# Kernel optimization log

Measured on AMD Instinct MI355X. Metric: run time of the kernel, lower is better.

Reference implementation:

```python
import jax, jax.numpy as jnp
from jax import lax
import numpy as np

R = 500          # Resampling: temporal segment width
H = 100          # fixed signal height from the reshape in forward
EPS = 1e-5       # BatchNorm2d default eps
FLAT = 6 * 31 * 32


def _cbrp(x, w, b, g, be, m, v):
    """Conv(5x5, pad 2) + inference BatchNorm + ReLU + MaxPool 2x2."""
    x = lax.conv_general_dilated(x, w, (1, 1), ((2, 2), (2, 2)),
                                 dimension_numbers=('NCHW', 'OIHW', 'NCHW'))
    x = x + b[None, :, None, None]
    inv = g * lax.rsqrt(v + EPS)
    x = x * inv[None, :, None, None] + (be - m * inv)[None, :, None, None]
    x = jax.nn.relu(x)
    return lax.reduce_window(x, -jnp.inf, lax.max, (1, 1, 2, 2), (1, 1, 2, 2), 'VALID')


def setup_inputs() -> dict:
    key = jax.random.key(0)
    ks = jax.random.split(key, 16)
    d = {}
    d['x'] = jax.random.normal(ks[0], (16, 1, 100, 4000), dtype=jnp.float32)
    chans = [(1, 16), (16, 32), (32, 64), (64, 32)]
    for i, (ci, co) in enumerate(chans, start=1):
        fan_in = ci * 25
        d[f'w{i}'] = jax.random.normal(ks[i], (co, ci, 5, 5), dtype=jnp.float32) * np.float32((2.0 / fan_in) ** 0.5)
        d[f'b{i}'] = jnp.zeros((co,), jnp.float32)
        d[f'g{i}'] = jnp.ones((co,), jnp.float32)
        d[f'be{i}'] = jnp.zeros((co,), jnp.float32)
        d[f'm{i}'] = jnp.zeros((co,), jnp.float32)
        d[f'v{i}'] = jnp.ones((co,), jnp.float32)
    d['fw1'] = jax.random.normal(ks[5], (32, FLAT), dtype=jnp.float32) * np.float32(FLAT ** -0.5)
    d['fb1'] = jnp.zeros((32,), jnp.float32)
    d['fw2'] = jax.random.normal(ks[6], (2, 32), dtype=jnp.float32) * np.float32(32 ** -0.5)
    d['fb2'] = jnp.zeros((2,), jnp.float32)
    return d


def reference(x, w1, b1, g1, be1, m1, v1,
              w2, b2, g2, be2, m2, v2,
              w3, b3, g3, be3, m3, v3,
              w4, b4, g4, be4, m4, v4,
              fw1, fb1, fw2, fb2):
    B = x.shape[0]
    L = x.shape[-1] // R  # number of temporal segments per sample
    # (B,1,100,L*R) -> (B*L,1,100,R): batch all segments into one conv call
    xs = x[:, 0].reshape(B, H, L, R).transpose(0, 2, 1, 3).reshape(B * L, 1, H, R)
    h = _cbrp(xs, w1, b1, g1, be1, m1, v1)   # (BL,16,50,250)
    h = _cbrp(h, w2, b2, g2, be2, m2, v2)    # (BL,32,25,125)
    h = _cbrp(h, w3, b3, g3, be3, m3, v3)    # (BL,64,12,62)
    h = _cbrp(h, w4, b4, g4, be4, m4, v4)    # (BL,32,6,31)
    h = h.reshape(B * L, FLAT)
    h = h @ fw1.T + fb1
    h = h @ fw2.T + fb2                      # (BL,2)
    return h.reshape(B, L, 2).mean(axis=1)   # average segment votes per sample
```

## Files before the change

### kernel.cpp

```cpp
#include <hip/hip_runtime.h>
#include <hip/hip_bf16.h>

#define EPSB 1e-5f

typedef short s16x8 __attribute__((ext_vector_type(8)));
typedef float f32x16 __attribute__((ext_vector_type(16)));

#define P1_OFF   0
#define P2_OFF   57507840
#define P3_OFF   89817088
#define L4_OFF   107642880
#define H1_OFF   110690304
#define WT2_OFF  110706688
#define WT3_OFF  110732288
#define WT4_OFF  110834688
#define SS2_OFF  110937088
#define SS3_OFF  110937344
#define SS4_OFF  110937856

__device__ __forceinline__ unsigned short bf16bits(float f) {
    __hip_bfloat16 h = __float2bfloat16(f);
    union { __hip_bfloat16 h; unsigned short u; } cv; cv.h = h; return cv.u;
}


template<int HP, int WP, int C, int IH, int IW>
__device__ __forceinline__ void pad_body(__hip_bfloat16* __restrict__ buf, int idx)
{
    if (idx >= 128 * HP * WP) return;
    const int rc = idx % (HP * WP);
    const int row = rc / WP, col = rc % WP;
    const bool pad = (row < 2) | (row >= 2 + IH) | (col < 2) | (col >= 2 + IW);
    if (!pad) return;
    int4* p = reinterpret_cast<int4*>(buf + (size_t)idx * C);
    #pragma unroll
    for (int i = 0; i < C * 2 / 16; ++i) p[i] = int4{0, 0, 0, 0};
}

__device__ __forceinline__ void wtrans_body(const float* __restrict__ src,
                                            __hip_bfloat16* __restrict__ dst,
                                            int CO, int CI, int idx)
{
    if (idx >= CO * CI * 25) return;
    const int co  = idx / (CI * 25);
    const int rem = idx % (CI * 25);
    const int ci  = rem / 25;
    const int tap = rem % 25;
    dst[((size_t)tap * CO + co) * CI + ci] = __float2bfloat16(src[idx]);
}

__device__ __forceinline__ void scsh_body(const float* __restrict__ b,
                                          const float* __restrict__ g,
                                          const float* __restrict__ be,
                                          const float* __restrict__ m,
                                          const float* __restrict__ v,
                                          float* __restrict__ out, int CO, int i)
{
    if (i < CO) {
        const float sc = g[i] * rsqrtf(v[i] + EPSB);
        out[i]      = sc;
        out[CO + i] = fmaf(b[i] - m[i], sc, be[i]);
    }
}

__global__ __launch_bounds__(256)
void prep_kernel(__hip_bfloat16* p1, __hip_bfloat16* p2, __hip_bfloat16* p3,
                 const float* w2, __hip_bfloat16* wt2,
                 const float* w3, __hip_bfloat16* wt3,
                 const float* w4, __hip_bfloat16* wt4,
                 const float* b2, const float* g2, const float* be2,
                 const float* m2, const float* v2, float* ss2,
                 const float* b3, const float* g3, const float* be3,
                 const float* m3, const float* v3, float* ss3,
                 const float* b4, const float* g4, const float* be4,
                 const float* m4, const float* v4, float* ss4)
{
    const int bid = blockIdx.x;
    const int tid = threadIdx.x;
    if      (bid < 7020) pad_body<54, 260, 16, 50, 250>(p1, bid * 256 + tid);
    else if (bid < 8992) pad_body<29, 136, 32, 25, 125>(p2, (bid - 7020) * 256 + tid);
    else if (bid < 9536) pad_body<16,  68, 64, 12,  62>(p3, (bid - 8992) * 256 + tid);
    else if (bid < 9586) wtrans_body(w2, wt2, 32, 16, (bid - 9536) * 256 + tid);
    else if (bid < 9786) wtrans_body(w3, wt3, 64, 32, (bid - 9586) * 256 + tid);
    else if (bid < 9986) wtrans_body(w4, wt4, 32, 64, (bid - 9786) * 256 + tid);
    else {
        const int which = bid - 9986;
        if      (which == 0) scsh_body(b2, g2, be2, m2, v2, ss2, 32, tid);
        else if (which == 1) scsh_body(b3, g3, be3, m3, v3, ss3, 64, tid);
        else                 scsh_body(b4, g4, be4, m4, v4, ss4, 32, tid);
    }
}

__global__ __launch_bounds__(256)
void conv1_kernel(const float* __restrict__ x,
                  const float* __restrict__ wgt,
                  const float* __restrict__ bias,
                  const float* __restrict__ g,
                  const float* __restrict__ be,
                  const float* __restrict__ m,
                  const float* __restrict__ v,
                  __hip_bfloat16* __restrict__ p1,
                  int n0)
{
    __shared__ float smem[6 * 504];
    const int n   = blockIdx.y + n0;
    const int ph  = blockIdx.x;
    const int tid = threadIdx.x;

    const int b = n >> 3, l = n & 7;
    const float* ib = x + (size_t)b * 400000 + l * 500;
    const int h0 = 2 * ph - 2;

    for (int i = tid; i < 6 * 504; i += 256) {
        const int rr = i / 504, cc = i % 504;
        const int hh = h0 + rr, ww = cc - 2;
        const bool ok = (hh >= 0) & (hh < 100) & (ww >= 0) & (ww < 500);
        smem[i] = ok ? ib[hh * 4000 + ww] : 0.0f;
    }
    __syncthreads();

    if (tid >= 250) return;
    const int pw = tid;

    float win[6][6];
    #pragma unroll
    for (int r = 0; r < 6; ++r)
        #pragma unroll
        for (int c = 0; c < 6; ++c)
            win[r][c] = smem[r * 504 + 2 * pw + c];

    int packed[8];
    #pragma unroll
    for (int cp = 0; cp < 8; ++cp) {
        unsigned short hb[2];
        #pragma unroll
        for (int sub = 0; sub < 2; ++sub) {
            const int co = 2 * cp + sub;
            float a0 = 0.f, a1 = 0.f, a2 = 0.f, a3 = 0.f;
            #pragma unroll
            for (int kh = 0; kh < 5; ++kh) {
                #pragma unroll
                for (int kw = 0; kw < 5; ++kw) {
                    const float w = wgt[co * 25 + kh * 5 + kw];
                    a0 = fmaf(w, win[kh  ][kw  ], a0);
                    a1 = fmaf(w, win[kh  ][kw+1], a1);
                    a2 = fmaf(w, win[kh+1][kw  ], a2);
                    a3 = fmaf(w, win[kh+1][kw+1], a3);
                }
            }
            const float sc = g[co] * rsqrtf(v[co] + EPSB);
            const float sh = fmaf(bias[co] - m[co], sc, be[co]);
            #define RA(a) fmaxf(fmaf((a), sc, sh), 0.0f)
            hb[sub] = bf16bits(fmaxf(fmaxf(RA(a0), RA(a1)), fmaxf(RA(a2), RA(a3))));
            #undef RA
        }
        packed[cp] = hb[0] | (hb[1] << 16);
    }

    int4* dst = reinterpret_cast<int4*>(
        p1 + (size_t)n * (54 * 260 * 16) + ((2 + ph) * 260 + (2 + pw)) * 16);
    dst[0] = int4{packed[0], packed[1], packed[2], packed[3]};
    dst[1] = int4{packed[4], packed[5], packed[6], packed[7]};
}

template<int CI, int CO, int HINP, int WINP, int HOUTP, int WOUTP,
         int PH, int PW, int NT, int NCOT, int RPW, bool NCHW_OUT>
__global__ __launch_bounds__(256)
void conv_mfma(const __hip_bfloat16* __restrict__ pin,
               const __hip_bfloat16* __restrict__ wq,
               const float* __restrict__ scsh,
               void* __restrict__ pout)
{
    constexpr int R = (PH + RPW - 1) / RPW;
    constexpr int NROW = 2 * RPW + 4;
    const int lane = threadIdx.x & 63;
    const int nbk  = gridDim.x;
    const int swz  = (blockIdx.x & 7) * (nbk >> 3) + (blockIdx.x >> 3);
    int t = swz * 4 + (threadIdx.x >> 6);
    const int cot = t % NCOT; t /= NCOT;
    const int wt  = t % NT;   t /= NT;
    const int r   = t % R;    t /= R;
    const int n   = t;
    if (n >= 128) return;

    const int lw = lane & 31, loct = lane >> 5;
    const int co0 = cot * 32;
    const int w0  = wt * 32;

    const __hip_bfloat16* bbase = pin + (size_t)n * (HINP * WINP * CI)
                                + (w0 + lw) * CI + loct * 8;
    const __hip_bfloat16* abase = wq + (co0 + lw) * CI + loct * 8;

    f32x16 acc[2 * RPW];
    #pragma unroll
    for (int q = 0; q < 2 * RPW; ++q) acc[q] = (f32x16){};

    #pragma unroll
    for (int kw = 0; kw < 5; ++kw) {
        #pragma unroll
        for (int s = 0; s < CI / 16; ++s) {
            s16x8 bfr[NROW];
            #pragma unroll
            for (int j = 0; j < NROW; ++j) {
                const int row = (2 * RPW * r + j < HINP) ? (2 * RPW * r + j) : (HINP - 1);
                bfr[j] = *reinterpret_cast<const s16x8*>(bbase + (row * WINP + kw) * CI + s * 16);
            }
            #pragma unroll
            for (int kh = 0; kh < 5; ++kh) {
                const s16x8 a = *reinterpret_cast<const s16x8*>(
                    abase + (size_t)((kh * 5 + kw) * CO) * CI + s * 16);
                #pragma unroll
                for (int q = 0; q < 2 * RPW; ++q)
                    acc[q] = __builtin_amdgcn_mfma_f32_32x32x16_bf16(a, bfr[kh + q], acc[q], 0, 0, 0);
            }
        }
    }

    const int pw = wt * 16 + (lw >> 1);
    const bool act = ((lane & 1) == 0) && (pw < PW);
    #pragma unroll
    for (int p = 0; p < RPW; ++p) {
        const int pr = RPW * r + p;
        const bool rok = (pr < PH);
        #pragma unroll
        for (int reg = 0; reg < 16; ++reg) {
            const int co = co0 + (reg & 3) + 8 * (reg >> 2) + 4 * loct;
            const float sc = scsh[co], sh = scsh[CO + co];
            const float v0 = fmaxf(fmaf(acc[2 * p    ][reg], sc, sh), 0.0f);
            const float v1 = fmaxf(fmaf(acc[2 * p + 1][reg], sc, sh), 0.0f);
            float vm = fmaxf(v0, v1);
            vm = fmaxf(vm, __shfl_xor(vm, 1, 64));
            if (act && rok) {
                if (NCHW_OUT) {
                    ((float*)pout)[(((size_t)n * CO + co) * PH + pr) * PW + pw] = vm;
                } else {
                    ((__hip_bfloat16*)pout)[(size_t)n * (HOUTP * WOUTP * CO)
                        + ((2 + pr) * WOUTP + (2 + pw)) * CO + co] = __float2bfloat16(vm);
                }
            }
        }
    }
}

__global__ __launch_bounds__(64)
void fc1_kernel(const float* __restrict__ h,
                const float* __restrict__ fw1,
                const float* __restrict__ fb1,
                float* __restrict__ h1)
{
    const int n = blockIdx.x;
    const int j = blockIdx.y;
    const int lane = threadIdx.x;
    const float* hp = h   + (size_t)n * 5952;
    const float* wp = fw1 + (size_t)j * 5952;
    float s = 0.0f;
    for (int k = lane; k < 5952; k += 64) s = fmaf(hp[k], wp[k], s);
    #pragma unroll
    for (int off = 32; off > 0; off >>= 1) s += __shfl_down(s, off, 64);
    if (lane == 0) h1[n * 32 + j] = s + fb1[j];
}

__global__ __launch_bounds__(64)
void fc2_mean_kernel(const float* __restrict__ h1,
                     const float* __restrict__ fw2,
                     const float* __restrict__ fb2,
                     float* __restrict__ out)
{
    const int t = threadIdx.x;
    if (t >= 32) return;
    const int b = t >> 1, c = t & 1;
    float s = 0.0f;
    for (int l = 0; l < 8; ++l) {
        const float* hp = h1 + (size_t)(b * 8 + l) * 32;
        #pragma unroll
        for (int j = 0; j < 32; ++j) s = fmaf(hp[j], fw2[c * 32 + j], s);
    }
    out[t] = fmaf(s, 0.125f, fb2[c]);
}

extern "C" void kernel_launch(void* const* d_in, const int* in_sizes, int n_in,
                              void* d_out, int out_size, void* d_ws, size_t ws_size,
                              hipStream_t stream)
{
    const float* x   = (const float*)d_in[0];
    const float* w1  = (const float*)d_in[1];
    const float* b1  = (const float*)d_in[2];
    const float* g1  = (const float*)d_in[3];
    const float* be1 = (const float*)d_in[4];
    const float* m1  = (const float*)d_in[5];
    const float* v1  = (const float*)d_in[6];
    const float* w2  = (const float*)d_in[7];
    const float* b2  = (const float*)d_in[8];
    const float* g2  = (const float*)d_in[9];
    const float* be2 = (const float*)d_in[10];
    const float* m2  = (const float*)d_in[11];
    const float* v2  = (const float*)d_in[12];
    const float* w3  = (const float*)d_in[13];
    const float* b3  = (const float*)d_in[14];
    const float* g3  = (const float*)d_in[15];
    const float* be3 = (const float*)d_in[16];
    const float* m3  = (const float*)d_in[17];
    const float* v3  = (const float*)d_in[18];
    const float* w4  = (const float*)d_in[19];
    const float* b4  = (const float*)d_in[20];
    const float* g4  = (const float*)d_in[21];
    const float* be4 = (const float*)d_in[22];
    const float* m4  = (const float*)d_in[23];
    const float* v4  = (const float*)d_in[24];
    const float* fw1 = (const float*)d_in[25];
    const float* fb1 = (const float*)d_in[26];
    const float* fw2 = (const float*)d_in[27];
    const float* fb2 = (const float*)d_in[28];

    char* ws = (char*)d_ws;
    __hip_bfloat16* p1  = (__hip_bfloat16*)(ws + P1_OFF);
    __hip_bfloat16* p2  = (__hip_bfloat16*)(ws + P2_OFF);
    __hip_bfloat16* p3  = (__hip_bfloat16*)(ws + P3_OFF);
    float*          l4  = (float*)(ws + L4_OFF);
    float*          h1  = (float*)(ws + H1_OFF);
    __hip_bfloat16* wt2 = (__hip_bfloat16*)(ws + WT2_OFF);
    __hip_bfloat16* wt3 = (__hip_bfloat16*)(ws + WT3_OFF);
    __hip_bfloat16* wt4 = (__hip_bfloat16*)(ws + WT4_OFF);
    float*          ss2 = (float*)(ws + SS2_OFF);
    float*          ss3 = (float*)(ws + SS3_OFF);
    float*          ss4 = (float*)(ws + SS4_OFF);

    prep_kernel<<<dim3(9989), 256, 0, stream>>>(
        p1, p2, p3, w2, wt2, w3, wt3, w4, wt4,
        b2, g2, be2, m2, v2, ss2,
        b3, g3, be3, m3, v3, ss3,
        b4, g4, be4, m4, v4, ss4);

    for (int c = 0; c < 4; ++c)
        conv1_kernel<<<dim3(50, 32), 256, 0, stream>>>(
            x, w1, b1, g1, be1, m1, v1, p1, c * 32);

    conv_mfma<16, 32, 54, 260, 29, 136, 25, 125, 8, 1, 4, false>
        <<<dim3(128 * 7 * 8 / 4), 256, 0, stream>>>(p1, wt2, ss2, p2);
    conv_mfma<32, 64, 29, 136, 16, 68, 12, 62, 4, 2, 4, false>
        <<<dim3(128 * 3 * 4 * 2 / 4), 256, 0, stream>>>(p2, wt3, ss3, p3);
    conv_mfma<64, 32, 16, 68, 0, 0, 6, 31, 2, 1, 2, true>
        <<<dim3(128 * 3 * 2 / 4), 256, 0, stream>>>(p3, wt4, ss4, l4);

    fc1_kernel<<<dim3(128, 32), 64, 0, stream>>>(l4, fw1, fb1, h1);
    fc2_mean_kernel<<<1, 64, 0, stream>>>(h1, fw2, fb2, (float*)d_out);
}
```

Before: 470.8 us.

## Stage conv2/conv3 input tiles in swizzled LDS shared across waves

Adds an MFMA conv kernel that cooperatively loads a block's input rows into XOR-swizzled shared memory, then has each wave read its B fragments from LDS instead of global memory. Waves in a block split width tiles and output-channel tiles, so neighbouring waves reuse the same staged input. Conv2 and conv3 switch to this kernel with two pooled rows per wave instead of four and a different grid. The aim is to cut redundant global/L2 reads of overlapping input windows, at the cost of a block barrier, LDS capacity pressure, and possibly lower per-wave accumulator reuse.

```diff
diff --git a/kernel.cpp b/kernel.cpp
--- a/kernel.cpp
+++ b/kernel.cpp
@@ -161,6 +161,108 @@
         p1 + (size_t)n * (54 * 260 * 16) + ((2 + ph) * 260 + (2 + pw)) * 16);
     dst[0] = int4{packed[0], packed[1], packed[2], packed[3]};
     dst[1] = int4{packed[4], packed[5], packed[6], packed[7]};
+}
+
+template<int CI, int CO, int HINP, int WINP, int HOUTP, int WOUTP,
+         int PH, int PW, int NT, int WTB, int COTB, bool NCHW_OUT>
+__global__ __launch_bounds__(256)
+void conv_mfma_lds(const __hip_bfloat16* __restrict__ pin,
+                   const __hip_bfloat16* __restrict__ wq,
+                   const float* __restrict__ scsh,
+                   void* __restrict__ pout)
+{
+    constexpr int RPW  = 2;
+    constexpr int R    = (PH + RPW - 1) / RPW;
+    constexpr int NROW = 2 * RPW + 4;
+    constexpr int GPW  = CI / 8;
+    constexpr int WST  = WTB * 32 + 8;
+    constexpr int GPR  = WST * GPW;
+    constexpr int WTG  = NT / WTB;
+    __shared__ short smem[NROW * GPR * 8];
+
+    const int nbk = gridDim.x;
+    const int swz = (blockIdx.x & 7) * (nbk >> 3) + (blockIdx.x >> 3);
+    int t = swz;
+    const int wtg = t % WTG; t /= WTG;
+    const int r   = t % R;   t /= R;
+    const int n   = t;
+
+    const int tid = threadIdx.x;
+    const int r0 = 2 * RPW * r;
+    const int w0blk = wtg * (WTB * 32);
+
+    for (int i = tid; i < NROW * GPR; i += 256) {
+        const int row_j = i / GPR;
+        const int gr    = i % GPR;
+        const int w = gr / GPW, gsub = gr % GPW;
+        int grow = r0 + row_j; if (grow > HINP - 1) grow = HINP - 1;
+        const size_t gaddr = (((size_t)n * HINP + grow) * WINP + (w0blk + w)) * CI + gsub * 8;
+        const s16x8 val = *reinterpret_cast<const s16x8*>(pin + gaddr);
+        const int Gp = i ^ ((i >> 3) & 7);
+        *reinterpret_cast<s16x8*>(&smem[Gp * 8]) = val;
+    }
+    __syncthreads();
+
+    const int wv = tid >> 6, lane = tid & 63;
+    const int lw = lane & 31, loct = lane >> 5;
+    const int wt_l = wv % WTB;
+    const int cot  = wv / WTB;
+    const int wt   = wtg * WTB + wt_l;
+    const int co0  = cot * 32;
+    const int w0l  = wt_l * 32;
+
+    const __hip_bfloat16* abase = wq + (co0 + lw) * CI + loct * 8;
+
+    f32x16 acc[4];
+    #pragma unroll
+    for (int q = 0; q < 4; ++q) acc[q] = (f32x16){};
+
+    #pragma unroll
+    for (int kw = 0; kw < 5; ++kw) {
+        #pragma unroll
+        for (int s = 0; s < CI / 16; ++s) {
+            s16x8 bfr[NROW];
+            #pragma unroll
+            for (int j = 0; j < NROW; ++j) {
+                int G = j * GPR + (w0l + lw + kw) * GPW + loct + 2 * s;
+                G ^= (G >> 3) & 7;
+                bfr[j] = *reinterpret_cast<const s16x8*>(&smem[G * 8]);
+            }
+            #pragma unroll
+            for (int kh = 0; kh < 5; ++kh) {
+                const s16x8 a = *reinterpret_cast<const s16x8*>(
+                    abase + (size_t)((kh * 5 + kw) * CO) * CI + s * 16);
+                #pragma unroll
+                for (int q = 0; q < 4; ++q)
+                    acc[q] = __builtin_amdgcn_mfma_f32_32x32x16_bf16(a, bfr[kh + q], acc[q], 0, 0, 0);
+            }
+        }
+    }
+
+    const int pw = wt * 16 + (lw >> 1);
+    const bool act = ((lane & 1) == 0) && (pw < PW);
+    #pragma unroll
+    for (int p = 0; p < RPW; ++p) {
+        const int pr = RPW * r + p;
+        const bool rok = (pr < PH);
+        #pragma unroll
+        for (int reg = 0; reg < 16; ++reg) {
+            const int co = co0 + (reg & 3) + 8 * (reg >> 2) + 4 * loct;
+            const float sc = scsh[co], sh = scsh[CO + co];
+            const float v0 = fmaxf(fmaf(acc[2 * p    ][reg], sc, sh), 0.0f);
+            const float v1 = fmaxf(fmaf(acc[2 * p + 1][reg], sc, sh), 0.0f);
+            float vm = fmaxf(v0, v1);
+            vm = fmaxf(vm, __shfl_xor(vm, 1, 64));
+            if (act && rok) {
+                if (NCHW_OUT) {
+                    ((float*)pout)[(((size_t)n * CO + co) * PH + pr) * PW + pw] = vm;
+                } else {
+                    ((__hip_bfloat16*)pout)[(size_t)n * (HOUTP * WOUTP * CO)
+                        + ((2 + pr) * WOUTP + (2 + pw)) * CO + co] = __float2bfloat16(vm);
+                }
+            }
+        }
+    }
 }
 
 template<int CI, int CO, int HINP, int WINP, int HOUTP, int WOUTP,
@@ -335,10 +437,10 @@
         conv1_kernel<<<dim3(50, 32), 256, 0, stream>>>(
             x, w1, b1, g1, be1, m1, v1, p1, c * 32);
 
-    conv_mfma<16, 32, 54, 260, 29, 136, 25, 125, 8, 1, 4, false>
-        <<<dim3(128 * 7 * 8 / 4), 256, 0, stream>>>(p1, wt2, ss2, p2);
-    conv_mfma<32, 64, 29, 136, 16, 68, 12, 62, 4, 2, 4, false>
-        <<<dim3(128 * 3 * 4 * 2 / 4), 256, 0, stream>>>(p2, wt3, ss3, p3);
+    conv_mfma_lds<16, 32, 54, 260, 29, 136, 25, 125, 8, 4, 1, false>
+        <<<dim3(128 * 13 * 2), 256, 0, stream>>>(p1, wt2, ss2, p2);
+    conv_mfma_lds<32, 64, 29, 136, 16, 68, 12, 62, 4, 2, 2, false>
+        <<<dim3(128 * 6 * 2), 256, 0, stream>>>(p2, wt3, ss3, p3);
     conv_mfma<64, 32, 16, 68, 0, 0, 6, 31, 2, 1, 2, true>
         <<<dim3(128 * 3 * 2 / 4), 256, 0, stream>>>(p3, wt4, ss4, l4);
 
```

New measurement: 448.9 us. -4.6%, faster.

## Compute one pooled row per wave and merge conv1 launches

Applied to the files above, without the earlier changes.

Each wave of the MFMA conv kernels now computes a single pooled output row (two conv rows) instead of RPW rows. This shrinks the accumulator set from 2*RPW to 2 and adds an occupancy hint of 4 blocks per CU. The grids grow accordingly, giving more waves and better latency hiding, but each wave reuses less from its loaded input rows and weight fragments. The four chunked conv1 launches are also folded into one launch covering all 128 segments, cutting launch overhead.

```diff
diff --git a/kernel.cpp b/kernel.cpp
--- a/kernel.cpp
+++ b/kernel.cpp
@@ -99,11 +99,10 @@
                   const float* __restrict__ be,
                   const float* __restrict__ m,
                   const float* __restrict__ v,
-                  __hip_bfloat16* __restrict__ p1,
-                  int n0)
+                  __hip_bfloat16* __restrict__ p1)
 {
     __shared__ float smem[6 * 504];
-    const int n   = blockIdx.y + n0;
+    const int n   = blockIdx.y;
     const int ph  = blockIdx.x;
     const int tid = threadIdx.x;
 
@@ -164,22 +163,21 @@
 }
 
 template<int CI, int CO, int HINP, int WINP, int HOUTP, int WOUTP,
-         int PH, int PW, int NT, int NCOT, int RPW, bool NCHW_OUT>
-__global__ __launch_bounds__(256)
+         int PH, int PW, int NT, int NCOT, bool NCHW_OUT>
+__global__ __launch_bounds__(256, 4)
 void conv_mfma(const __hip_bfloat16* __restrict__ pin,
                const __hip_bfloat16* __restrict__ wq,
                const float* __restrict__ scsh,
                void* __restrict__ pout)
 {
-    constexpr int R = (PH + RPW - 1) / RPW;
-    constexpr int NROW = 2 * RPW + 4;
+    constexpr int NROW = 6;
     const int lane = threadIdx.x & 63;
     const int nbk  = gridDim.x;
     const int swz  = (blockIdx.x & 7) * (nbk >> 3) + (blockIdx.x >> 3);
     int t = swz * 4 + (threadIdx.x >> 6);
     const int cot = t % NCOT; t /= NCOT;
     const int wt  = t % NT;   t /= NT;
-    const int r   = t % R;    t /= R;
+    const int r   = t % PH;   t /= PH;
     const int n   = t;
     if (n >= 128) return;
 
@@ -191,9 +189,8 @@
                                 + (w0 + lw) * CI + loct * 8;
     const __hip_bfloat16* abase = wq + (co0 + lw) * CI + loct * 8;
 
-    f32x16 acc[2 * RPW];
-    #pragma unroll
-    for (int q = 0; q < 2 * RPW; ++q) acc[q] = (f32x16){};
+    f32x16 acc0 = {};
+    f32x16 acc1 = {};
 
     #pragma unroll
     for (int kw = 0; kw < 5; ++kw) {
@@ -202,16 +199,15 @@
             s16x8 bfr[NROW];
             #pragma unroll
             for (int j = 0; j < NROW; ++j) {
-                const int row = (2 * RPW * r + j < HINP) ? (2 * RPW * r + j) : (HINP - 1);
+                const int row = 2 * r + j;
                 bfr[j] = *reinterpret_cast<const s16x8*>(bbase + (row * WINP + kw) * CI + s * 16);
             }
             #pragma unroll
             for (int kh = 0; kh < 5; ++kh) {
                 const s16x8 a = *reinterpret_cast<const s16x8*>(
                     abase + (size_t)((kh * 5 + kw) * CO) * CI + s * 16);
-                #pragma unroll
-                for (int q = 0; q < 2 * RPW; ++q)
-                    acc[q] = __builtin_amdgcn_mfma_f32_32x32x16_bf16(a, bfr[kh + q], acc[q], 0, 0, 0);
+                acc0 = __builtin_amdgcn_mfma_f32_32x32x16_bf16(a, bfr[kh],     acc0, 0, 0, 0);
+                acc1 = __builtin_amdgcn_mfma_f32_32x32x16_bf16(a, bfr[kh + 1], acc1, 0, 0, 0);
             }
         }
     }
@@ -219,24 +215,19 @@
     const int pw = wt * 16 + (lw >> 1);
     const bool act = ((lane & 1) == 0) && (pw < PW);
     #pragma unroll
-    for (int p = 0; p < RPW; ++p) {
-        const int pr = RPW * r + p;
-        const bool rok = (pr < PH);
-        #pragma unroll
-        for (int reg = 0; reg < 16; ++reg) {
-            const int co = co0 + (reg & 3) + 8 * (reg >> 2) + 4 * loct;
-            const float sc = scsh[co], sh = scsh[CO + co];
-            const float v0 = fmaxf(fmaf(acc[2 * p    ][reg], sc, sh), 0.0f);
-            const float v1 = fmaxf(fmaf(acc[2 * p + 1][reg], sc, sh), 0.0f);
-            float vm = fmaxf(v0, v1);
-            vm = fmaxf(vm, __shfl_xor(vm, 1, 64));
-            if (act && rok) {
-                if (NCHW_OUT) {
-                    ((float*)pout)[(((size_t)n * CO + co) * PH + pr) * PW + pw] = vm;
-                } else {
-                    ((__hip_bfloat16*)pout)[(size_t)n * (HOUTP * WOUTP * CO)
-                        + ((2 + pr) * WOUTP + (2 + pw)) * CO + co] = __float2bfloat16(vm);
-                }
+    for (int reg = 0; reg < 16; ++reg) {
+        const int co = co0 + (reg & 3) + 8 * (reg >> 2) + 4 * loct;
+        const float sc = scsh[co], sh = scsh[CO + co];
+        const float v0 = fmaxf(fmaf(acc0[reg], sc, sh), 0.0f);
+        const float v1 = fmaxf(fmaf(acc1[reg], sc, sh), 0.0f);
+        float vm = fmaxf(v0, v1);
+        vm = fmaxf(vm, __shfl_xor(vm, 1, 64));
+        if (act) {
+            if (NCHW_OUT) {
+                ((float*)pout)[(((size_t)n * CO + co) * PH + r) * PW + pw] = vm;
+            } else {
+                ((__hip_bfloat16*)pout)[(size_t)n * (HOUTP * WOUTP * CO)
+                    + ((2 + r) * WOUTP + (2 + pw)) * CO + co] = __float2bfloat16(vm);
             }
         }
     }
@@ -331,16 +322,14 @@
         b3, g3, be3, m3, v3, ss3,
         b4, g4, be4, m4, v4, ss4);
 
-    for (int c = 0; c < 4; ++c)
-        conv1_kernel<<<dim3(50, 32), 256, 0, stream>>>(
-            x, w1, b1, g1, be1, m1, v1, p1, c * 32);
-
-    conv_mfma<16, 32, 54, 260, 29, 136, 25, 125, 8, 1, 4, false>
-        <<<dim3(128 * 7 * 8 / 4), 256, 0, stream>>>(p1, wt2, ss2, p2);
-    conv_mfma<32, 64, 29, 136, 16, 68, 12, 62, 4, 2, 4, false>
-        <<<dim3(128 * 3 * 4 * 2 / 4), 256, 0, stream>>>(p2, wt3, ss3, p3);
-    conv_mfma<64, 32, 16, 68, 0, 0, 6, 31, 2, 1, 2, true>
-        <<<dim3(128 * 3 * 2 / 4), 256, 0, stream>>>(p3, wt4, ss4, l4);
+    conv1_kernel<<<dim3(50, 128), 256, 0, stream>>>(x, w1, b1, g1, be1, m1, v1, p1);
+
+    conv_mfma<16, 32, 54, 260, 29, 136, 25, 125, 8, 1, false>
+        <<<dim3(128 * 25 * 8 / 4), 256, 0, stream>>>(p1, wt2, ss2, p2);
+    conv_mfma<32, 64, 29, 136, 16, 68, 12, 62, 4, 2, false>
+        <<<dim3(128 * 12 * 4 * 2 / 4), 256, 0, stream>>>(p2, wt3, ss3, p3);
+    conv_mfma<64, 32, 16, 68, 0, 0, 6, 31, 2, 1, true>
+        <<<dim3(128 * 6 * 2 / 4), 256, 0, stream>>>(p3, wt4, ss4, l4);
 
     fc1_kernel<<<dim3(128, 32), 64, 0, stream>>>(l4, fw1, fb1, h1);
     fc2_mean_kernel<<<1, 64, 0, stream>>>(h1, fw2, fb2, (float*)d_out);
```

Measured after the change: 479.1 us. No clear change (+1.8%).
